# Kernel tuning notes

Hardware: AMD Instinct MI355X
Metric: run time of the kernel (lower is better)

Reference implementation:

```python
import jax, jax.numpy as jnp
import numpy as np

N, D, V = 4096, 256, 32000
B, T = 32, 256
U_DECAY, X_DECAY = 0.97, 0.97
EPS = 1e-6


def layernorm_row(z):
    # matches torch: (z - mean) / (std + eps), std with Bessel correction (ddof=1)
    m = jnp.mean(z, axis=-1, keepdims=True)
    s = jnp.std(z, axis=-1, keepdims=True, ddof=1)
    return (z - m) / (s + EPS)


def setup_inputs() -> dict:
    key = jax.random.key(0)
    k1, k2, k3, k4, k5 = jax.random.split(key, 5)
    token_emb = jax.random.normal(k1, (V, D), jnp.float32) / np.float32(np.sqrt(D))
    E = jax.random.normal(k2, (D, N), jnp.float32) / np.float32(np.sqrt(N))
    Dx = jax.random.normal(k3, (N, D), jnp.float32) / np.float32(np.sqrt(D))
    Dy = jax.random.normal(k4, (N, D), jnp.float32) / np.float32(np.sqrt(D))
    idx = jax.random.randint(k5, (B, T), 0, V)
    return {"idx": idx, "token_emb": token_emb, "E": E, "Dx": Dx, "Dy": Dy}


def reference(idx, token_emb, E, Dx, Dy):
    b = idx.shape[0]

    def step(carry, tok):
        x, rho = carry                                   # x: (b,n), rho: (b,d,n)
        v_prev = token_emb[tok]                          # (b,d) embedding gather
        x_t = X_DECAY * x + jax.nn.relu(v_prev @ Dx.T)   # (b,n)
        x_t = x_t / (jnp.sum(jnp.abs(x_t), axis=-1, keepdims=True) + EPS)  # L1 normalize
        a_star = jnp.einsum('bdn,bn->bd', rho, x_t)      # fast-weight readout
        y_t = jax.nn.relu(layernorm_row(a_star) @ Dy.T) * jax.nn.relu(x_t)  # (b,n)
        v_star = layernorm_row(y_t @ E.T)                # (b,d)
        # Hebbian decayed outer-product memory update
        rho = U_DECAY * (rho + jnp.einsum('bd,bn->bdn', layernorm_row(v_prev), x_t))
        return (x_t, rho), v_star

    x0 = jnp.zeros((b, N), jnp.float32)
    rho0 = jnp.zeros((b, D, N), jnp.float32)
    (_, _), vs = jax.lax.scan(step, (x0, rho0), idx.T)   # vs: (T,b,d)
    return jnp.transpose(vs, (1, 0, 2))                  # (b,T,d)
```

## Files before the change

### kernel.cpp

```cpp
#include <hip/hip_runtime.h>
#include <hip/hip_bf16.h>

#define NN 4096
#define DD 256
#define BB 32
#define TT 256
#define EPS 1e-6f
#define DECAY 0.97f
#define LOG2_DECAY -0.043943348f

typedef __hip_bfloat16 bf16;
typedef short short8 __attribute__((ext_vector_type(8)));
typedef float floatx4 __attribute__((ext_vector_type(4)));

__device__ __forceinline__ float bfu2f(short u) {
    return __uint_as_float(((unsigned)(unsigned short)u) << 16);
}

__device__ __forceinline__ float blk_sum_256(float v, volatile float* s4) {
#pragma unroll
    for (int o = 32; o > 0; o >>= 1) v += __shfl_down(v, o, 64);
    int lane = threadIdx.x & 63, w = threadIdx.x >> 6;
    __syncthreads();
    if (lane == 0) s4[w] = v;
    __syncthreads();
    return s4[0] + s4[1] + s4[2] + s4[3];
}

__device__ __forceinline__ void gl16(const bf16* g, bf16* l) {
    __builtin_amdgcn_global_load_lds((const __attribute__((address_space(1))) void*)g,
                                     (__attribute__((address_space(3))) void*)l, 16, 0, 0);
}

__global__ void k_detect(const unsigned short* __restrict__ raw, int* __restrict__ flag) {
    __shared__ int cnt[4];
    int tid = threadIdx.x;
    int bad = 0;
    for (int i = tid; i < 8192; i += 256) {
        unsigned int u = raw[2 * i];
        float v = __uint_as_float(u << 16);
        if (!(fabsf(v) < 1e6f)) bad++;
    }
#pragma unroll
    for (int o = 32; o > 0; o >>= 1) bad += __shfl_down(bad, o, 64);
    int lane = tid & 63, w = tid >> 6;
    if (lane == 0) cnt[w] = bad;
    __syncthreads();
    if (tid == 0) flag[0] = (cnt[0] + cnt[1] + cnt[2] + cnt[3] < 32) ? 1 : 0;
}

__global__ __launch_bounds__(256) void k_convert3(const void* __restrict__ s0,
                                                  const void* __restrict__ s1,
                                                  const void* __restrict__ s2,
                                                  bf16* __restrict__ d0,
                                                  bf16* __restrict__ d1,
                                                  bf16* __restrict__ d2,
                                                  const int* __restrict__ flag) {
    const int per = NN * DD / 8;
    int i = blockIdx.x * 256 + threadIdx.x;
    int m = i / per, j = i % per;
    const void* s = (m == 0) ? s0 : (m == 1) ? s1 : s2;
    bf16* d = (m == 0) ? d0 : (m == 1) ? d1 : d2;
    if (flag[0]) {
        ((uint4*)d)[j] = ((const uint4*)s)[j];
    } else {
        const float4* f = (const float4*)s;
        float4 a = f[2 * j], b = f[2 * j + 1];
        short8 o;
        float va[8] = {a.x, a.y, a.z, a.w, b.x, b.y, b.z, b.w};
#pragma unroll
        for (int k = 0; k < 8; k++) {
            bf16 t = __float2bfloat16(va[k]);
            o[k] = *reinterpret_cast<short*>(&t);
        }
        ((short8*)d)[j] = o;
    }
}

__global__ __launch_bounds__(256) void k_gather_ln(const void* __restrict__ emb,
                                                   const int* __restrict__ idx,
                                                   bf16* __restrict__ Vpb,
                                                   bf16* __restrict__ Ub,
                                                   const int* __restrict__ flag) {
    __shared__ float s4[4];
    int r = blockIdx.x, d = threadIdx.x;
    int tok = idx[r];
    long o = (long)tok * DD + d;
    float e = flag[0] ? __bfloat162float(((const bf16*)emb)[o]) : ((const float*)emb)[o];
    Vpb[(long)r * DD + d] = __float2bfloat16(e);
    float m = blk_sum_256(e, s4) * (1.0f / DD);
    float zc = e - m;
    float var = blk_sum_256(zc * zc, s4) * (1.0f / (DD - 1));
    Ub[(long)r * DD + d] = __float2bfloat16(zc / (sqrtf(fmaxf(var, 0.f)) + EPS));
}

__global__ __launch_bounds__(256) void k_transpose(const bf16* __restrict__ Ub,
                                                   bf16* __restrict__ Ut) {
    __shared__ bf16 tile[32][33];
    int b = blockIdx.z;
    int t0 = blockIdx.x * 32, d0 = blockIdx.y * 32;
    const bf16* src = Ub + (long)b * TT * DD;
    bf16* dst = Ut + (long)b * DD * TT;
    int rr = threadIdx.x >> 3, c4 = (threadIdx.x & 7) * 4;
#pragma unroll
    for (int i = 0; i < 4; i++) tile[rr][c4 + i] = src[(long)(t0 + rr) * DD + d0 + c4 + i];
    __syncthreads();
#pragma unroll
    for (int i = 0; i < 4; i++) dst[(long)(d0 + rr) * TT + t0 + c4 + i] = tile[c4 + i][rr];
}

enum { EPI_RELU_BF16 = 0, EPI_NONE_F32 = 1, EPI_RELU_MULX_BF16 = 2 };

template <int EPI, int KSPLIT, int TRI>
__global__ __launch_bounds__(256) void k_mfma_nt(int K,
                                                 const bf16* __restrict__ A, int lda, long sA,
                                                 const bf16* __restrict__ B, int ldb, long sB,
                                                 void* __restrict__ Cv, int ldc, long sC,
                                                 const bf16* __restrict__ Xaux,
                                                 float* __restrict__ Wsum) {
    __shared__ __align__(16) char smem[32768];
    bf16* R = (bf16*)smem;

    int z = blockIdx.z;
    int bz = z / KSPLIT, ks = z % KSPLIT;
    A += (long)bz * sA;
    B += (long)bz * sB;
    int bx = blockIdx.x, by = blockIdx.y;
    if (TRI) {
        by = (blockIdx.x >= 1) ? 1 : 0;
        bx = (blockIdx.x == 2) ? 1 : 0;
    }
    int bm = by * 128, bn = bx * 128;
    int tid = threadIdx.x;
    int srow = tid >> 2;
    int scol = ((((srow >> 1) & 3) ^ (tid & 3)) << 3);
    int w = tid >> 6, lane = tid & 63;
    int wm = (w >> 1) * 64, wn = (w & 1) * 64;
    int lm = lane & 15, kh = lane >> 4;

    floatx4 acc[4][4];
#pragma unroll
    for (int i = 0; i < 4; i++)
#pragma unroll
        for (int j = 0; j < 4; j++) acc[i][j] = (floatx4){0.f, 0.f, 0.f, 0.f};

    int kchunk = K / KSPLIT;
    int kbeg = ks * kchunk, kend = kbeg + kchunk;
    const bf16* gA0 = A + (long)(bm + srow) * lda + scol;
    const bf16* gA1 = gA0 + (long)64 * lda;
    const bf16* gB0 = B + (long)(bn + srow) * ldb + scol;
    const bf16* gB1 = gB0 + (long)64 * ldb;
    int dslot = tid * 8;

    {
        bf16* bufA = (bf16*)smem;
        bf16* bufB = bufA + 4096;
        gl16(gA0 + kbeg, bufA + dslot);
        gl16(gA1 + kbeg, bufA + 2048 + dslot);
        gl16(gB0 + kbeg, bufB + dslot);
        gl16(gB1 + kbeg, bufB + 2048 + dslot);
    }
    __syncthreads();

    int cur = 0;
    for (int k0 = kbeg; k0 < kend; k0 += 32) {
        bf16* cbA = (bf16*)(smem + (cur ? 16384 : 0));
        bf16* cbB = cbA + 4096;
        bf16* nbA = (bf16*)(smem + (cur ? 0 : 16384));
        bf16* nbB = nbA + 4096;
        if (k0 + 32 < kend) {
            gl16(gA0 + k0 + 32, nbA + dslot);
            gl16(gA1 + k0 + 32, nbA + 2048 + dslot);
            gl16(gB0 + k0 + 32, nbB + dslot);
            gl16(gB1 + k0 + 32, nbB + 2048 + dslot);
        }
        short8 af[4], bfr[4];
#pragma unroll
        for (int i = 0; i < 4; i++) {
            int row = wm + i * 16 + lm;
            af[i] = *(const short8*)(cbA + row * 32 + ((((row >> 1) & 3) ^ kh) << 3));
        }
#pragma unroll
        for (int j = 0; j < 4; j++) {
            int row = wn + j * 16 + lm;
            bfr[j] = *(const short8*)(cbB + row * 32 + ((((row >> 1) & 3) ^ kh) << 3));
        }
#pragma unroll
        for (int i = 0; i < 4; i++)
#pragma unroll
            for (int j = 0; j < 4; j++)
                acc[i][j] = __builtin_amdgcn_mfma_f32_16x16x32_bf16(af[i], bfr[j], acc[i][j], 0, 0, 0);
        __syncthreads();
        cur ^= 1;
    }

    if (EPI == EPI_NONE_F32) {
        long cbase = (long)z * sC;
#pragma unroll
        for (int i = 0; i < 4; i++)
#pragma unroll
            for (int j = 0; j < 4; j++)
#pragma unroll
                for (int r = 0; r < 4; r++) {
                    int gm = bm + wm + i * 16 + kh * 4 + r;
                    int gn = bn + wn + j * 16 + lm;
                    ((float*)Cv)[cbase + (long)gm * ldc + gn] = acc[i][j][r];
                }
        return;
    }

#pragma unroll
    for (int p = 0; p < 2; p++) {
        __syncthreads();
        if ((w >> 1) == p) {
#pragma unroll
            for (int i = 0; i < 4; i++)
#pragma unroll
                for (int j = 0; j < 4; j++)
#pragma unroll
                    for (int r = 0; r < 4; r++) {
                        int rr = i * 16 + kh * 4 + r;
                        int cc = wn + j * 16 + lm;
                        R[rr * 136 + cc] = __float2bfloat16(fmaxf(acc[i][j][r], 0.f));
                    }
        }
        __syncthreads();
#pragma unroll
        for (int it = 0; it < 4; it++) {
            int row_l = it * 16 + (tid >> 4);
            int c8 = (tid & 15) * 8;
            short8 vv = *(const short8*)(R + row_l * 136 + c8);
            int gm = bm + p * 64 + row_l;
            long off = (long)gm * ldc + bn + c8;
            if (EPI == EPI_RELU_BF16) {
                *(short8*)((bf16*)Cv + off) = vv;
                float s = 0.f;
#pragma unroll
                for (int k = 0; k < 8; k++) s += bfu2f(vv[k]);
#pragma unroll
                for (int o = 8; o > 0; o >>= 1) s += __shfl_down(s, o, 16);
                if ((tid & 15) == 0) atomicAdd(&Wsum[gm], s);
            } else {
                short8 xx = *(const short8*)(Xaux + off);
                short8 oo;
#pragma unroll
                for (int k = 0; k < 8; k++) {
                    float prod = bfu2f(vv[k]) * fmaxf(bfu2f(xx[k]), 0.f);
                    bf16 t = __float2bfloat16(prod);
                    oo[k] = *reinterpret_cast<short*>(&t);
                }
                *(short8*)((bf16*)Cv + off) = oo;
            }
        }
    }
}

__global__ __launch_bounds__(256) void k_scalar_scan(const float* __restrict__ Wsum,
                                                     float* __restrict__ invS) {
    __shared__ float sw[BB * TT];
    for (int i = threadIdx.x; i < BB * TT; i += 256) sw[i] = Wsum[i];
    __syncthreads();
    int b = threadIdx.x;
    if (b < BB) {
        float sig = 0.f;
        for (int t = 0; t < TT; t++) {
            float S = DECAY * sig + sw[b * TT + t];
            float inv = 1.f / (S + EPS);
            invS[b * TT + t] = inv;
            sig = S * inv;
        }
    }
}

__global__ __launch_bounds__(256) void k_colscan(bf16* __restrict__ W,
                                                 const float* __restrict__ invS) {
    __shared__ float sv[TT];
    int b = blockIdx.y;
    sv[threadIdx.x] = invS[b * TT + threadIdx.x];
    __syncthreads();
    int n = blockIdx.x * 256 + threadIdx.x;
    bf16* p = W + (long)b * TT * NN + n;
    float x = 0.f;
    for (int t = 0; t < TT; t++) {
        float w = __bfloat162float(p[(long)t * NN]);
        x = (DECAY * x + w) * sv[t];
        p[(long)t * NN] = __float2bfloat16(x);
    }
}

__global__ __launch_bounds__(256) void k_reduce_mask(const float* __restrict__ Gp,
                                                     bf16* __restrict__ G) {
    int r = blockIdx.x;
    int b = r >> 8, t = r & 255;
    int s = threadIdx.x;
    long base = ((long)b * 4) * 65536 + (long)t * 256 + s;
    float v = Gp[base] + Gp[base + 65536] + Gp[base + 2 * 65536] + Gp[base + 3 * 65536];
    float o = (s < t) ? v * exp2f((float)(t - s) * LOG2_DECAY) : 0.f;
    G[(long)r * 256 + s] = __float2bfloat16(o);
}

__global__ __launch_bounds__(256) void k_ln_rows(const float* __restrict__ Zp,
                                                 bf16* __restrict__ O) {
    __shared__ float s4[4];
    long r = blockIdx.x;
    int d = threadIdx.x;
    long b = r >> 8, t = r & 255;
    long base = (b * 2) * 65536 + t * 256 + d;
    float z = Zp[base] + Zp[base + 65536];
    float m = blk_sum_256(z, s4) * (1.0f / DD);
    float zc = z - m;
    float var = blk_sum_256(zc * zc, s4) * (1.0f / (DD - 1));
    O[r * DD + d] = __float2bfloat16(zc / (sqrtf(fmaxf(var, 0.f)) + EPS));
}

__global__ __launch_bounds__(256) void k_final_ln(const float* __restrict__ Zp,
                                                  void* __restrict__ out,
                                                  const int* __restrict__ flag) {
    __shared__ float s4[4];
    long r = blockIdx.x;
    int d = threadIdx.x;
    const long SL = (long)8192 * 256;
    long o = r * DD + d;
    float z = Zp[o] + Zp[o + SL] + Zp[o + 2 * SL] + Zp[o + 3 * SL];
    float m = blk_sum_256(z, s4) * (1.0f / DD);
    float zc = z - m;
    float var = blk_sum_256(zc * zc, s4) * (1.0f / (DD - 1));
    float v = zc / (sqrtf(fmaxf(var, 0.f)) + EPS);
    if (flag[0]) ((bf16*)out)[o] = __float2bfloat16(v);
    else ((float*)out)[o] = v;
}

extern "C" void kernel_launch(void* const* d_in, const int* in_sizes, int n_in,
                              void* d_out, int out_size, void* d_ws, size_t ws_size,
                              hipStream_t stream) {
    const int* idx = (const int*)d_in[0];
    const void* emb = d_in[1];
    const void* E = d_in[2];
    const void* Dx = d_in[3];
    const void* Dy = d_in[4];

    char* base = (char*)d_ws;
    size_t off = 0;
    int* flag = (int*)base; off += 1024;
    bf16* Dxb = (bf16*)(base + off); off += (size_t)NN * DD * 2;
    bf16* Dyb = (bf16*)(base + off); off += (size_t)NN * DD * 2;
    bf16* Eb  = (bf16*)(base + off); off += (size_t)DD * NN * 2;
    bf16* Vpb = (bf16*)(base + off); off += (size_t)BB * TT * DD * 2;
    bf16* Ub  = (bf16*)(base + off); off += (size_t)BB * TT * DD * 2;
    bf16* Ut  = (bf16*)(base + off); off += (size_t)BB * TT * DD * 2;
    float* Wsum = (float*)(base + off); off += (size_t)BB * TT * 4;
    float* invS = (float*)(base + off); off += (size_t)BB * TT * 4;
    bf16* ALNb = (bf16*)(base + off); off += (size_t)BB * TT * DD * 2;
    bf16* G = (bf16*)(base + off); off += (size_t)BB * TT * TT * 2;
    float* Gp = (float*)(base + off); off += (size_t)4 * BB * TT * TT * 4;
    float* Astar = Gp;
    float* Zp = Gp;
    bf16* Xb = (bf16*)(base + off); off += (size_t)BB * TT * NN * 2;

    const int M = BB * TT;

    k_detect<<<1, 256, 0, stream>>>((const unsigned short*)emb, flag);
    k_convert3<<<3 * NN * DD / 8 / 256, 256, 0, stream>>>(Dx, Dy, E, Dxb, Dyb, Eb, flag);
    k_gather_ln<<<M, 256, 0, stream>>>(emb, idx, Vpb, Ub, flag);
    k_transpose<<<dim3(8, 8, BB), 256, 0, stream>>>(Ub, Ut);

    hipMemsetAsync(Wsum, 0, (size_t)M * 4, stream);

    k_mfma_nt<EPI_RELU_BF16, 1, 0><<<dim3(32, 64, 1), 256, 0, stream>>>(
        DD, Vpb, DD, 0, Dxb, DD, 0, Xb, NN, 0, nullptr, Wsum);

    k_scalar_scan<<<1, 256, 0, stream>>>(Wsum, invS);
    k_colscan<<<dim3(16, BB, 1), 256, 0, stream>>>(Xb, invS);

    k_mfma_nt<EPI_NONE_F32, 4, 1><<<dim3(3, 1, BB * 4), 256, 0, stream>>>(
        NN, Xb, NN, (long)TT * NN, Xb, NN, (long)TT * NN, Gp, TT, (long)TT * TT, nullptr, nullptr);
    k_reduce_mask<<<M, 256, 0, stream>>>(Gp, G);

    k_mfma_nt<EPI_NONE_F32, 2, 0><<<dim3(2, 2, BB * 2), 256, 0, stream>>>(
        TT, G, TT, (long)TT * TT, Ut, TT, (long)DD * TT, Astar, DD, (long)TT * DD, nullptr, nullptr);
    k_ln_rows<<<M, 256, 0, stream>>>(Astar, ALNb);

    k_mfma_nt<EPI_RELU_MULX_BF16, 1, 0><<<dim3(32, 64, 1), 256, 0, stream>>>(
        DD, ALNb, DD, 0, Dyb, DD, 0, Xb, NN, 0, Xb, nullptr);

    k_mfma_nt<EPI_NONE_F32, 4, 0><<<dim3(2, 64, 4), 256, 0, stream>>>(
        NN, Xb, NN, 0, Eb, NN, 0, Zp, DD, (long)M * DD, nullptr, nullptr);

    k_final_ln<<<M, 256, 0, stream>>>(Zp, d_out, flag);
}
```

Baseline: 319.4 us.

## Triple-buffer GEMM K-loop with vmcnt waits and add XCD-aware block swizzle

Replaces the double-buffered shared-memory pipeline in the MFMA GEMM with a three-stage ring. Loads run two K-steps ahead and explicit s_waitcnt vmcnt counts wait only for the stage about to be consumed, with raw barriers in place of __syncthreads. It also adds an optional workgroup-ID remap that groups every eighth block, aimed at L2 locality across the MI355X's chiplets, and enables it for three of the GEMM launches. The cost is LDS growing from 32KB to 48KB per block, which may reduce occupancy. The hand-written vmcnt values also depend on the exact count of outstanding global loads, which is fragile.

```diff
diff --git a/kernel.cpp b/kernel.cpp
--- a/kernel.cpp
+++ b/kernel.cpp
@@ -111,14 +111,14 @@
 
 enum { EPI_RELU_BF16 = 0, EPI_NONE_F32 = 1, EPI_RELU_MULX_BF16 = 2 };
 
-template <int EPI, int KSPLIT, int TRI>
+template <int EPI, int KSPLIT, int TRI, int SWZ>
 __global__ __launch_bounds__(256) void k_mfma_nt(int K,
                                                  const bf16* __restrict__ A, int lda, long sA,
                                                  const bf16* __restrict__ B, int ldb, long sB,
                                                  void* __restrict__ Cv, int ldc, long sC,
                                                  const bf16* __restrict__ Xaux,
                                                  float* __restrict__ Wsum) {
-    __shared__ __align__(16) char smem[32768];
+    __shared__ __align__(16) char smem[49152];
     bf16* R = (bf16*)smem;
 
     int z = blockIdx.z;
@@ -130,6 +130,15 @@
         by = (blockIdx.x >= 1) ? 1 : 0;
         bx = (blockIdx.x == 2) ? 1 : 0;
     }
+    if (SWZ) {
+        int gx = gridDim.x;
+        int nwg = gx * gridDim.y;
+        int id = by * gx + bx;
+        int q = nwg >> 3;
+        int nid = (id & 7) * q + (id >> 3);
+        bx = nid % gx;
+        by = nid / gx;
+    }
     int bm = by * 128, bn = bx * 128;
     int tid = threadIdx.x;
     int srow = tid >> 2;
@@ -152,28 +161,35 @@
     const bf16* gB1 = gB0 + (long)64 * ldb;
     int dslot = tid * 8;
 
-    {
-        bf16* bufA = (bf16*)smem;
-        bf16* bufB = bufA + 4096;
-        gl16(gA0 + kbeg, bufA + dslot);
-        gl16(gA1 + kbeg, bufA + 2048 + dslot);
-        gl16(gB0 + kbeg, bufB + dslot);
-        gl16(gB1 + kbeg, bufB + 2048 + dslot);
-    }
-    __syncthreads();
+#define STAGE_SLOT(SBASE, KK)                          \
+    {                                                  \
+        bf16* bufA = (bf16*)(SBASE);                   \
+        bf16* bufB = bufA + 4096;                      \
+        gl16(gA0 + (KK), bufA + dslot);                \
+        gl16(gA1 + (KK), bufA + 2048 + dslot);         \
+        gl16(gB0 + (KK), bufB + dslot);                \
+        gl16(gB1 + (KK), bufB + 2048 + dslot);         \
+    }
+
+    STAGE_SLOT(smem, kbeg);
+    if (kbeg + 32 < kend) STAGE_SLOT(smem + 16384, kbeg + 32);
 
     int cur = 0;
     for (int k0 = kbeg; k0 < kend; k0 += 32) {
-        bf16* cbA = (bf16*)(smem + (cur ? 16384 : 0));
+        __builtin_amdgcn_s_barrier();
+        __builtin_amdgcn_sched_barrier(0);
+        if (k0 + 64 < kend) {
+            int ps = (cur == 0) ? 2 : cur - 1;
+            STAGE_SLOT(smem + ps * 16384, k0 + 64);
+        }
+        int rem = (kend - k0 - 32) >> 5;
+        if (rem >= 2)      asm volatile("s_waitcnt vmcnt(8)" ::: "memory");
+        else if (rem == 1) asm volatile("s_waitcnt vmcnt(4)" ::: "memory");
+        else               asm volatile("s_waitcnt vmcnt(0)" ::: "memory");
+        __builtin_amdgcn_s_barrier();
+        __builtin_amdgcn_sched_barrier(0);
+        bf16* cbA = (bf16*)(smem + cur * 16384);
         bf16* cbB = cbA + 4096;
-        bf16* nbA = (bf16*)(smem + (cur ? 0 : 16384));
-        bf16* nbB = nbA + 4096;
-        if (k0 + 32 < kend) {
-            gl16(gA0 + k0 + 32, nbA + dslot);
-            gl16(gA1 + k0 + 32, nbA + 2048 + dslot);
-            gl16(gB0 + k0 + 32, nbB + dslot);
-            gl16(gB1 + k0 + 32, nbB + 2048 + dslot);
-        }
         short8 af[4], bfr[4];
 #pragma unroll
         for (int i = 0; i < 4; i++) {
@@ -190,9 +206,9 @@
 #pragma unroll
             for (int j = 0; j < 4; j++)
                 acc[i][j] = __builtin_amdgcn_mfma_f32_16x16x32_bf16(af[i], bfr[j], acc[i][j], 0, 0, 0);
-        __syncthreads();
-        cur ^= 1;
-    }
+        cur = (cur == 2) ? 0 : cur + 1;
+    }
+#undef STAGE_SLOT
 
     if (EPI == EPI_NONE_F32) {
         long cbase = (long)z * sC;
@@ -366,24 +382,24 @@
 
     hipMemsetAsync(Wsum, 0, (size_t)M * 4, stream);
 
-    k_mfma_nt<EPI_RELU_BF16, 1, 0><<<dim3(32, 64, 1), 256, 0, stream>>>(
+    k_mfma_nt<EPI_RELU_BF16, 1, 0, 1><<<dim3(32, 64, 1), 256, 0, stream>>>(
         DD, Vpb, DD, 0, Dxb, DD, 0, Xb, NN, 0, nullptr, Wsum);
 
     k_scalar_scan<<<1, 256, 0, stream>>>(Wsum, invS);
     k_colscan<<<dim3(16, BB, 1), 256, 0, stream>>>(Xb, invS);
 
-    k_mfma_nt<EPI_NONE_F32, 4, 1><<<dim3(3, 1, BB * 4), 256, 0, stream>>>(
+    k_mfma_nt<EPI_NONE_F32, 4, 1, 0><<<dim3(3, 1, BB * 4), 256, 0, stream>>>(
         NN, Xb, NN, (long)TT * NN, Xb, NN, (long)TT * NN, Gp, TT, (long)TT * TT, nullptr, nullptr);
     k_reduce_mask<<<M, 256, 0, stream>>>(Gp, G);
 
-    k_mfma_nt<EPI_NONE_F32, 2, 0><<<dim3(2, 2, BB * 2), 256, 0, stream>>>(
+    k_mfma_nt<EPI_NONE_F32, 2, 0, 0><<<dim3(2, 2, BB * 2), 256, 0, stream>>>(
         TT, G, TT, (long)TT * TT, Ut, TT, (long)DD * TT, Astar, DD, (long)TT * DD, nullptr, nullptr);
     k_ln_rows<<<M, 256, 0, stream>>>(Astar, ALNb);
 
-    k_mfma_nt<EPI_RELU_MULX_BF16, 1, 0><<<dim3(32, 64, 1), 256, 0, stream>>>(
+    k_mfma_nt<EPI_RELU_MULX_BF16, 1, 0, 1><<<dim3(32, 64, 1), 256, 0, stream>>>(
         DD, ALNb, DD, 0, Dyb, DD, 0, Xb, NN, 0, Xb, nullptr);
 
-    k_mfma_nt<EPI_NONE_F32, 4, 0><<<dim3(2, 64, 4), 256, 0, stream>>>(
+    k_mfma_nt<EPI_NONE_F32, 4, 0, 1><<<dim3(2, 64, 4), 256, 0, stream>>>(
         NN, Xb, NN, 0, Eb, NN, 0, Zp, DD, (long)M * DD, nullptr, nullptr);
 
     k_final_ln<<<M, 256, 0, stream>>>(Zp, d_out, flag);
```

Measured after the change: 310.2 us. 1.03x faster.
